# Kernel optimization log

Hardware: AMD Instinct MI355X
Metric: run time of the kernel (lower is better)

## Reference

```python
import jax, jax.numpy as jnp
import numpy as np


def squash(x, axis=-1):
    # norm_sq/(1+norm_sq) * x/norm, exactly as the torch version
    norm_sq = jnp.sum(x * x, axis=axis, keepdims=True)
    norm = jnp.sqrt(norm_sq)
    return norm_sq / (1.0 + norm_sq) * (x / norm)


def setup_inputs() -> dict:
    key = jax.random.key(0)
    k1, k2 = jax.random.split(key)
    batch, in_caps, in_hid, out_caps, out_hid = 128, 1152, 16, 32, 16
    input_capsules = jax.random.normal(k1, (batch, in_caps, in_hid), dtype=jnp.float32)
    # EinMix weight: 'in_caps in_hid out_caps out_hid'
    W = jax.random.normal(k2, (in_caps, in_hid, out_caps, out_hid), dtype=jnp.float32) * 0.05
    return {"input_capsules": input_capsules, "W": W, "routing_iterations": 3}


def reference(input_capsules, W, routing_iterations):
    # U: [batch, in_caps, out_caps, out_hid]
    U = jnp.einsum('bih,ihoj->bioj', input_capsules, W)
    batch, in_caps, out_caps, out_hid = U.shape
    B = jnp.zeros((batch, in_caps, out_caps), dtype=U.dtype)
    V = None
    for _ in range(routing_iterations):
        C = jax.nn.softmax(B, axis=-1)           # [b, i, o]
        S = jnp.einsum('bio,bioh->boh', C, U)    # [b, o, h]
        V = squash(S, axis=-1)                   # [b, o, h]
        B = B + jnp.einsum('bioh,boh->bio', U, V)
    return V
```

## Files before the change

### kernel.cpp

```cpp
#include <hip/hip_runtime.h>
#include <hip/hip_bf16.h>


#define IN_CAPS 1152
#define OUT_CAPS 32
#define BATCH 128
#define IPC 16
#define NBLK_I (IN_CAPS / IPC)
#define SV_ELEMS (BATCH * OUT_CAPS * 16)

typedef __attribute__((ext_vector_type(8))) short short8;
typedef __attribute__((ext_vector_type(4))) float f32x4;

__device__ inline unsigned f2bf(float x) {
  unsigned u = __builtin_bit_cast(unsigned, x);
  return (u + 0x7FFFu + ((u >> 16) & 1u)) >> 16;
}

__global__ __launch_bounds__(256) void conv_w(const float* __restrict__ W,
                                              unsigned short* __restrict__ Wb) {
  const int tid = blockIdx.x * 256 + threadIdx.x;
  const int l = tid & 31;
  const int o = (tid >> 5) & 31;
  const int i = tid >> 10;
  const int k0 = (l >> 4) * 8;
  const int c = o * 16 + (l & 15);
  const float* src = W + ((size_t)i * 16 + k0) * 512 + c;
  unsigned b[8];
#pragma unroll
  for (int j = 0; j < 8; ++j) b[j] = f2bf(src[(size_t)j * 512]);
  uint4 out;
  out.x = b[0] | (b[1] << 16);
  out.y = b[2] | (b[3] << 16);
  out.z = b[4] | (b[5] << 16);
  out.w = b[6] | (b[7] << 16);
  *(uint4*)(Wb + (size_t)tid * 8) = out;
}

__global__ __launch_bounds__(256) void conv_x(const float* __restrict__ X,
                                              unsigned short* __restrict__ xa) {
  const int tid = blockIdx.x * 256 + threadIdx.x;
  const int l = tid & 63;
  const int r = tid >> 6;
  const int i = r % IN_CAPS;
  const int bg = r / IN_CAPS;
  uint4 out = make_uint4(0, 0, 0, 0);
  if (l < 32) {
    const int b = bg * 16 + (l & 15);
    const int k0 = (l >> 4) * 8;
    const float* src = X + ((size_t)b * IN_CAPS + i) * 16 + k0;
    float4 a = ((const float4*)src)[0];
    float4 c = ((const float4*)src)[1];
    out.x = f2bf(a.x) | (f2bf(a.y) << 16);
    out.y = f2bf(a.z) | (f2bf(a.w) << 16);
    out.z = f2bf(c.x) | (f2bf(c.y) << 16);
    out.w = f2bf(c.z) | (f2bf(c.w) << 16);
  }
  *(uint4*)(xa + (size_t)tid * 8) = out;
}

template <int PASS>
__global__ __launch_bounds__(512, 4)
void caps_pass(const unsigned short* __restrict__ Wb,
               const unsigned short* __restrict__ xa,
               const float* __restrict__ Vt,
               float* __restrict__ P) {
  __shared__ float part[2][8][16];

  const int t = threadIdx.x, w = t >> 6, l = t & 63;
  const int q = l >> 4, bl = l & 15;
  const int bg = blockIdx.y, iblk = blockIdx.x, i0 = iblk * IPC;

  const short8* wp = (const short8*)Wb + ((size_t)i0 * 32 + w * 4) * 32 + (l & 31);
  const short8* xp = (const short8*)xa + ((size_t)bg * IN_CAPS + i0) * 64 + l;

  f32x4 sacc[4];
  f32x4 v[4];
#pragma unroll
  for (int m = 0; m < 4; ++m) {
    sacc[m] = (f32x4){0.f, 0.f, 0.f, 0.f};
    if constexpr (PASS == 2)
      v[m] = ((const f32x4*)Vt)[((size_t)(bg * 8 + w) * 64 + l) * 4 + m];
  }

  for (int ii = 0; ii < IPC; ++ii) {
    short8 a[4];
    if (l < 32) {
#pragma unroll
      for (int m = 0; m < 4; ++m) a[m] = wp[m * 32];
    } else {
#pragma unroll
      for (int m = 0; m < 4; ++m) a[m] = (short8){0, 0, 0, 0, 0, 0, 0, 0};
    }
    wp += 1024;
    short8 x = *xp;
    xp += 64;

    if constexpr (PASS == 1) {
#pragma unroll
      for (int m = 0; m < 4; ++m)
        sacc[m] = __builtin_amdgcn_mfma_f32_16x16x32_bf16(a[m], x, sacc[m], 0, 0, 0);
    } else {
      const f32x4 z = {0.f, 0.f, 0.f, 0.f};
      f32x4 d[4];
#pragma unroll
      for (int m = 0; m < 4; ++m)
        d[m] = __builtin_amdgcn_mfma_f32_16x16x32_bf16(a[m], x, z, 0, 0, 0);

      float e[4], esum;
#pragma unroll
      for (int m = 0; m < 4; ++m) {
        f32x4 pr = d[m] * v[m];
        float p = (pr[0] + pr[1]) + (pr[2] + pr[3]);
        p += __shfl_xor(p, 16);
        p += __shfl_xor(p, 32);
        e[m] = __expf(p);
      }
      esum = (e[0] + e[1]) + (e[2] + e[3]);
      if (q == 0) part[ii & 1][w][bl] = esum;
      __syncthreads();
      float den = 0.f;
#pragma unroll
      for (int ww = 0; ww < 8; ++ww) den += part[ii & 1][ww][bl];
      const float rden = __builtin_amdgcn_rcpf(den);
#pragma unroll
      for (int m = 0; m < 4; ++m) sacc[m] += d[m] * (e[m] * rden);
    }
  }

  float* pp = P + ((size_t)iblk * 128 + bg * 16 + bl) * 512 + w * 64 + q * 4;
#pragma unroll
  for (int m = 0; m < 4; ++m) {
    f32x4 val = sacc[m];
    if constexpr (PASS == 1) val *= (1.f / 32.f);
    *(f32x4*)(pp + m * 16) = val;
  }
}

template <int MODE>
__global__ __launch_bounds__(256)
void reduce_squash(const float* __restrict__ P, const float* __restrict__ V1,
                   float* __restrict__ Vt, float* __restrict__ V1out,
                   float* __restrict__ Out) {
  const int j = blockIdx.x * 256 + threadIdx.x;
  float s = 0.f;
  const float* p = P + j;
#pragma unroll 8
  for (int k = 0; k < NBLK_I; ++k) s += p[(size_t)k * SV_ELEMS];
  float ns = s * s;
  ns += __shfl_xor(ns, 1);
  ns += __shfl_xor(ns, 2);
  ns += __shfl_xor(ns, 4);
  ns += __shfl_xor(ns, 8);
  const float sc = ns / ((1.f + ns) * sqrtf(ns));
  float vv = s * sc;
  if constexpr (MODE == 2) {
    Out[j] = vv;
  } else {
    if constexpr (MODE == 0) V1out[j] = vv;
    if constexpr (MODE == 1) vv += V1[j];
    const int b = j >> 9, oh = j & 511, o = oh >> 4, h = oh & 15;
    const int bg = b >> 4, bl = b & 15, w = o >> 2, m = o & 3, qq = h >> 2;
    Vt[(((size_t)(bg * 8 + w) * 64 + qq * 16 + bl) * 16) + m * 4 + (h & 3)] = vv;
  }
}

extern "C" void kernel_launch(void* const* d_in, const int* in_sizes, int n_in,
                              void* d_out, int out_size, void* d_ws, size_t ws_size,
                              hipStream_t stream) {
  const float* X  = (const float*)d_in[0];
  const float* Wg = (const float*)d_in[1];

  float* P   = (float*)d_ws;
  float* Vt  = P + (size_t)NBLK_I * SV_ELEMS;
  float* V1p = Vt + SV_ELEMS;
  unsigned short* Wb = (unsigned short*)(V1p + SV_ELEMS);
  unsigned short* xa = Wb + (size_t)IN_CAPS * 32 * 32 * 8;
  float* out = (float*)d_out;

  conv_w<<<(IN_CAPS * 32 * 32) / 256, 256, 0, stream>>>(Wg, Wb);
  conv_x<<<(8 * IN_CAPS * 64) / 256, 256, 0, stream>>>(X, xa);

  const dim3 grid(NBLK_I, 8);
  const dim3 blk(512);

  caps_pass<1><<<grid, blk, 0, stream>>>(Wb, xa, nullptr, P);
  reduce_squash<0><<<256, 256, 0, stream>>>(P, nullptr, Vt, V1p, nullptr);

  caps_pass<2><<<grid, blk, 0, stream>>>(Wb, xa, Vt, P);
  reduce_squash<1><<<256, 256, 0, stream>>>(P, V1p, Vt, nullptr, nullptr);

  caps_pass<2><<<grid, blk, 0, stream>>>(Wb, xa, Vt, P);
  reduce_squash<2><<<256, 256, 0, stream>>>(P, nullptr, nullptr, nullptr, out);
}
```

Baseline: 181.3 us.

## Fuse input bf16 conversion into routing passes and retile to 512 blocks

Removes the separate conv_x kernel and instead has each routing-pass block convert its slice of X to bf16 directly into shared memory. conv_w now stages W through shared memory so both reads and writes are coalesced. IPC changes from 16 to 18 and the grid becomes a 1-D 512-block launch, so blocks line up with the CU count. Pass 2/3 also software-prefetches the next W and x fragments. The aim is to cut one launch and the bf16 x round-trip through global memory, at the cost of redundant per-pass conversion work and extra LDS use.

Result: faster. 165.1 us (-8.9%).

```diff
diff --git a/kernel.cpp b/kernel.cpp
--- a/kernel.cpp
+++ b/kernel.cpp
@@ -5,7 +5,7 @@
 #define IN_CAPS 1152
 #define OUT_CAPS 32
 #define BATCH 128
-#define IPC 16
+#define IPC 18
 #define NBLK_I (IN_CAPS / IPC)
 #define SV_ELEMS (BATCH * OUT_CAPS * 16)
 
@@ -19,129 +19,165 @@
 
 __global__ __launch_bounds__(256) void conv_w(const float* __restrict__ W,
                                               unsigned short* __restrict__ Wb) {
-  const int tid = blockIdx.x * 256 + threadIdx.x;
-  const int l = tid & 31;
-  const int o = (tid >> 5) & 31;
-  const int i = tid >> 10;
-  const int k0 = (l >> 4) * 8;
-  const int c = o * 16 + (l & 15);
-  const float* src = W + ((size_t)i * 16 + k0) * 512 + c;
-  unsigned b[8];
-#pragma unroll
-  for (int j = 0; j < 8; ++j) b[j] = f2bf(src[(size_t)j * 512]);
-  uint4 out;
-  out.x = b[0] | (b[1] << 16);
-  out.y = b[2] | (b[3] << 16);
-  out.z = b[4] | (b[5] << 16);
-  out.w = b[6] | (b[7] << 16);
-  *(uint4*)(Wb + (size_t)tid * 8) = out;
-}
-
-__global__ __launch_bounds__(256) void conv_x(const float* __restrict__ X,
-                                              unsigned short* __restrict__ xa) {
-  const int tid = blockIdx.x * 256 + threadIdx.x;
-  const int l = tid & 63;
-  const int r = tid >> 6;
-  const int i = r % IN_CAPS;
-  const int bg = r / IN_CAPS;
-  uint4 out = make_uint4(0, 0, 0, 0);
-  if (l < 32) {
-    const int b = bg * 16 + (l & 15);
-    const int k0 = (l >> 4) * 8;
-    const float* src = X + ((size_t)b * IN_CAPS + i) * 16 + k0;
-    float4 a = ((const float4*)src)[0];
-    float4 c = ((const float4*)src)[1];
-    out.x = f2bf(a.x) | (f2bf(a.y) << 16);
-    out.y = f2bf(a.z) | (f2bf(a.w) << 16);
-    out.z = f2bf(c.x) | (f2bf(c.y) << 16);
-    out.w = f2bf(c.z) | (f2bf(c.w) << 16);
-  }
-  *(uint4*)(xa + (size_t)tid * 8) = out;
-}
-
-template <int PASS>
+  __shared__ float st[16 * 516];
+  const int t = threadIdx.x;
+  const size_t ibase = (size_t)blockIdx.x * 8192;
+  const float4* src = (const float4*)(W + ibase);
+#pragma unroll
+  for (int r = 0; r < 8; ++r) {
+    const int f = r * 256 + t;
+    const int k = f >> 7, c4 = f & 127;
+    *(float4*)&st[k * 516 + c4 * 4] = src[f];
+  }
+  __syncthreads();
+  unsigned short* dst = Wb + ibase;
+#pragma unroll
+  for (int r = 0; r < 4; ++r) {
+    const int u = r * 256 + t;
+    const int o = u >> 5, l = u & 31;
+    const int col = o * 16 + (l & 15), k0 = (l >> 4) * 8;
+    unsigned b[8];
+#pragma unroll
+    for (int j = 0; j < 8; ++j) b[j] = f2bf(st[(k0 + j) * 516 + col]);
+    uint4 outv;
+    outv.x = b[0] | (b[1] << 16);
+    outv.y = b[2] | (b[3] << 16);
+    outv.z = b[4] | (b[5] << 16);
+    outv.w = b[6] | (b[7] << 16);
+    *(uint4*)(dst + (size_t)u * 8) = outv;
+  }
+}
+
+__device__ __forceinline__ void build_xs(const float* __restrict__ X, int bg,
+                                         int i0, int t, unsigned (*xs)[64][4]) {
+#pragma unroll
+  for (int rep = 0; rep < IPC * 256 / 512; ++rep) {
+    const int base = rep * 512 + t;
+    const int ii = base >> 8;
+    const int e = base & 255;
+    const int l2 = e >> 2, ju = e & 3;
+    unsigned val = 0;
+    if (l2 < 32) {
+      const float2 f = *(const float2*)(X +
+          ((size_t)(bg * 16 + (l2 & 15)) * IN_CAPS + (i0 + ii)) * 16 +
+          (l2 >> 4) * 8 + 2 * ju);
+      val = f2bf(f.x) | (f2bf(f.y) << 16);
+    }
+    xs[ii][l2][ju] = val;
+  }
+}
+
+__device__ __forceinline__ short8 ld_x(const unsigned (*xs)[64][4], int ii, int l) {
+  return __builtin_bit_cast(short8, *(const uint4*)(&xs[ii][l][0]));
+}
+
 __global__ __launch_bounds__(512, 4)
-void caps_pass(const unsigned short* __restrict__ Wb,
-               const unsigned short* __restrict__ xa,
-               const float* __restrict__ Vt,
-               float* __restrict__ P) {
-  __shared__ float part[2][8][16];
-
+void caps_pass1(const unsigned short* __restrict__ Wb,
+                const float* __restrict__ X, float* __restrict__ P) {
+  __shared__ __align__(16) unsigned xs[IPC][64][4];
   const int t = threadIdx.x, w = t >> 6, l = t & 63;
   const int q = l >> 4, bl = l & 15;
-  const int bg = blockIdx.y, iblk = blockIdx.x, i0 = iblk * IPC;
+  const int gx = blockIdx.x, iblk = gx & 63, bg = gx >> 6;
+  const int i0 = iblk * IPC;
+
+  build_xs(X, bg, i0, t, xs);
+  __syncthreads();
 
   const short8* wp = (const short8*)Wb + ((size_t)i0 * 32 + w * 4) * 32 + (l & 31);
-  const short8* xp = (const short8*)xa + ((size_t)bg * IN_CAPS + i0) * 64 + l;
-
   f32x4 sacc[4];
-  f32x4 v[4];
+#pragma unroll
+  for (int m = 0; m < 4; ++m) sacc[m] = (f32x4){0.f, 0.f, 0.f, 0.f};
+
+  for (int ii = 0; ii < IPC; ++ii) {
+    short8 x = ld_x(xs, ii, l);
+    short8 a0 = wp[0], a1 = wp[32], a2 = wp[64], a3 = wp[96];
+    wp += 1024;
+    sacc[0] = __builtin_amdgcn_mfma_f32_16x16x32_bf16(a0, x, sacc[0], 0, 0, 0);
+    sacc[1] = __builtin_amdgcn_mfma_f32_16x16x32_bf16(a1, x, sacc[1], 0, 0, 0);
+    sacc[2] = __builtin_amdgcn_mfma_f32_16x16x32_bf16(a2, x, sacc[2], 0, 0, 0);
+    sacc[3] = __builtin_amdgcn_mfma_f32_16x16x32_bf16(a3, x, sacc[3], 0, 0, 0);
+  }
+  float* pp = P + ((size_t)iblk * 128 + bg * 16 + bl) * 512 + w * 64 + q * 4;
+#pragma unroll
+  for (int m = 0; m < 4; ++m) *(f32x4*)(pp + m * 16) = sacc[m] * (1.f / 32.f);
+}
+
+__global__ __launch_bounds__(512, 4)
+void caps_pass23(const unsigned short* __restrict__ Wb,
+                 const float* __restrict__ X,
+                 const float* __restrict__ Vt,
+                 float* __restrict__ P) {
+  __shared__ __align__(16) unsigned xs[IPC][64][4];
+  __shared__ float part[2][8][16];
+  const int t = threadIdx.x, w = t >> 6, l = t & 63;
+  const int q = l >> 4, bl = l & 15;
+  const int gx = blockIdx.x, iblk = gx & 63, bg = gx >> 6;
+  const int i0 = iblk * IPC;
+
+  f32x4 v[4], sacc[4];
 #pragma unroll
   for (int m = 0; m < 4; ++m) {
+    v[m] = ((const f32x4*)Vt)[((size_t)(bg * 8 + w) * 64 + l) * 4 + m];
     sacc[m] = (f32x4){0.f, 0.f, 0.f, 0.f};
-    if constexpr (PASS == 2)
-      v[m] = ((const f32x4*)Vt)[((size_t)(bg * 8 + w) * 64 + l) * 4 + m];
-  }
+  }
+
+  build_xs(X, bg, i0, t, xs);
+  __syncthreads();
+
+  const short8* wp = (const short8*)Wb + ((size_t)i0 * 32 + w * 4) * 32 + (l & 31);
+  short8 an[4];
+  short8 xn = ld_x(xs, 0, l);
+#pragma unroll
+  for (int m = 0; m < 4; ++m) an[m] = wp[m * 32];
+  wp += 1024;
 
   for (int ii = 0; ii < IPC; ++ii) {
-    short8 a[4];
-    if (l < 32) {
-#pragma unroll
-      for (int m = 0; m < 4; ++m) a[m] = wp[m * 32];
-    } else {
-#pragma unroll
-      for (int m = 0; m < 4; ++m) a[m] = (short8){0, 0, 0, 0, 0, 0, 0, 0};
+    short8 ac[4];
+#pragma unroll
+    for (int m = 0; m < 4; ++m) ac[m] = an[m];
+    short8 xc = xn;
+    if (ii + 1 < IPC) {
+      xn = ld_x(xs, ii + 1, l);
+#pragma unroll
+      for (int m = 0; m < 4; ++m) an[m] = wp[m * 32];
+      wp += 1024;
     }
-    wp += 1024;
-    short8 x = *xp;
-    xp += 64;
-
-    if constexpr (PASS == 1) {
-#pragma unroll
-      for (int m = 0; m < 4; ++m)
-        sacc[m] = __builtin_amdgcn_mfma_f32_16x16x32_bf16(a[m], x, sacc[m], 0, 0, 0);
-    } else {
-      const f32x4 z = {0.f, 0.f, 0.f, 0.f};
-      f32x4 d[4];
-#pragma unroll
-      for (int m = 0; m < 4; ++m)
-        d[m] = __builtin_amdgcn_mfma_f32_16x16x32_bf16(a[m], x, z, 0, 0, 0);
-
-      float e[4], esum;
-#pragma unroll
-      for (int m = 0; m < 4; ++m) {
-        f32x4 pr = d[m] * v[m];
-        float p = (pr[0] + pr[1]) + (pr[2] + pr[3]);
-        p += __shfl_xor(p, 16);
-        p += __shfl_xor(p, 32);
-        e[m] = __expf(p);
-      }
-      esum = (e[0] + e[1]) + (e[2] + e[3]);
-      if (q == 0) part[ii & 1][w][bl] = esum;
-      __syncthreads();
-      float den = 0.f;
-#pragma unroll
-      for (int ww = 0; ww < 8; ++ww) den += part[ii & 1][ww][bl];
-      const float rden = __builtin_amdgcn_rcpf(den);
-#pragma unroll
-      for (int m = 0; m < 4; ++m) sacc[m] += d[m] * (e[m] * rden);
+
+    const f32x4 z = {0.f, 0.f, 0.f, 0.f};
+    f32x4 d[4];
+#pragma unroll
+    for (int m = 0; m < 4; ++m)
+      d[m] = __builtin_amdgcn_mfma_f32_16x16x32_bf16(ac[m], xc, z, 0, 0, 0);
+
+    float e[4];
+#pragma unroll
+    for (int m = 0; m < 4; ++m) {
+      f32x4 pr = d[m] * v[m];
+      float p = (pr[0] + pr[1]) + (pr[2] + pr[3]);
+      p += __shfl_xor(p, 16);
+      p += __shfl_xor(p, 32);
+      e[m] = __expf(p);
     }
+    const float esum = (e[0] + e[1]) + (e[2] + e[3]);
+    if (q == 0) part[ii & 1][w][bl] = esum;
+    __syncthreads();
+    float den = 0.f;
+#pragma unroll
+    for (int ww = 0; ww < 8; ++ww) den += part[ii & 1][ww][bl];
+    const float rden = __builtin_amdgcn_rcpf(den);
+#pragma unroll
+    for (int m = 0; m < 4; ++m) sacc[m] += d[m] * (e[m] * rden);
   }
 
   float* pp = P + ((size_t)iblk * 128 + bg * 16 + bl) * 512 + w * 64 + q * 4;
 #pragma unroll
-  for (int m = 0; m < 4; ++m) {
-    f32x4 val = sacc[m];
-    if constexpr (PASS == 1) val *= (1.f / 32.f);
-    *(f32x4*)(pp + m * 16) = val;
-  }
+  for (int m = 0; m < 4; ++m) *(f32x4*)(pp + m * 16) = sacc[m];
 }
 
 template <int MODE>
 __global__ __launch_bounds__(256)
-void reduce_squash(const float* __restrict__ P, const float* __restrict__ V1,
-                   float* __restrict__ Vt, float* __restrict__ V1out,
-                   float* __restrict__ Out) {
+void reduce_squash(const float* __restrict__ P, float* __restrict__ Vt,
+                   float* __restrict__ V1p, float* __restrict__ Out) {
   const int j = blockIdx.x * 256 + threadIdx.x;
   float s = 0.f;
   const float* p = P + j;
@@ -157,8 +193,8 @@
   if constexpr (MODE == 2) {
     Out[j] = vv;
   } else {
-    if constexpr (MODE == 0) V1out[j] = vv;
-    if constexpr (MODE == 1) vv += V1[j];
+    if constexpr (MODE == 0) V1p[j] = vv;
+    if constexpr (MODE == 1) vv += V1p[j];
     const int b = j >> 9, oh = j & 511, o = oh >> 4, h = oh & 15;
     const int bg = b >> 4, bl = b & 15, w = o >> 2, m = o & 3, qq = h >> 2;
     Vt[(((size_t)(bg * 8 + w) * 64 + qq * 16 + bl) * 16) + m * 4 + (h & 3)] = vv;
@@ -175,21 +211,16 @@
   float* Vt  = P + (size_t)NBLK_I * SV_ELEMS;
   float* V1p = Vt + SV_ELEMS;
   unsigned short* Wb = (unsigned short*)(V1p + SV_ELEMS);
-  unsigned short* xa = Wb + (size_t)IN_CAPS * 32 * 32 * 8;
   float* out = (float*)d_out;
 
-  conv_w<<<(IN_CAPS * 32 * 32) / 256, 256, 0, stream>>>(Wg, Wb);
-  conv_x<<<(8 * IN_CAPS * 64) / 256, 256, 0, stream>>>(X, xa);
-
-  const dim3 grid(NBLK_I, 8);
-  const dim3 blk(512);
-
-  caps_pass<1><<<grid, blk, 0, stream>>>(Wb, xa, nullptr, P);
-  reduce_squash<0><<<256, 256, 0, stream>>>(P, nullptr, Vt, V1p, nullptr);
-
-  caps_pass<2><<<grid, blk, 0, stream>>>(Wb, xa, Vt, P);
-  reduce_squash<1><<<256, 256, 0, stream>>>(P, V1p, Vt, nullptr, nullptr);
-
-  caps_pass<2><<<grid, blk, 0, stream>>>(Wb, xa, Vt, P);
-  reduce_squash<2><<<256, 256, 0, stream>>>(P, nullptr, nullptr, nullptr, out);
-}
+  conv_w<<<IN_CAPS, 256, 0, stream>>>(Wg, Wb);
+
+  caps_pass1<<<512, 512, 0, stream>>>(Wb, X, P);
+  reduce_squash<0><<<256, 256, 0, stream>>>(P, Vt, V1p, nullptr);
+
+  caps_pass23<<<512, 512, 0, stream>>>(Wb, X, Vt, P);
+  reduce_squash<1><<<256, 256, 0, stream>>>(P, Vt, V1p, nullptr);
+
+  caps_pass23<<<512, 512, 0, stream>>>(Wb, X, Vt, P);
+  reduce_squash<2><<<256, 256, 0, stream>>>(P, nullptr, nullptr, out);
+}
```
